# Kernel tuning notes

Measured on AMD Instinct MI355X. Metric: run time of the kernel, lower is better.

Reference implementation:

```python
import jax, jax.numpy as jnp
import numpy as np

IN_DIM = 128
OUT_DIM = 128
NUM_HEADS = 4
HEAD_DIM = OUT_DIM // NUM_HEADS  # 32
B, N = 4, 4096


def setup_inputs() -> dict:
    key = jax.random.key(0)
    ks = jax.random.split(key, 7)
    s_in = 1.0 / np.sqrt(IN_DIM)
    s_out = 1.0 / np.sqrt(OUT_DIM)
    return {
        "x": jax.random.normal(ks[0], (B, N, IN_DIM), dtype=jnp.float32),
        "adjacency": jax.random.randint(ks[1], (N, N), 0, 2, dtype=jnp.int32),
        "W_q": jax.random.uniform(ks[2], (IN_DIM, NUM_HEADS * HEAD_DIM), jnp.float32, -s_in, s_in),
        "W_k": jax.random.uniform(ks[3], (IN_DIM, NUM_HEADS * HEAD_DIM), jnp.float32, -s_in, s_in),
        "W_v": jax.random.uniform(ks[4], (IN_DIM, NUM_HEADS * HEAD_DIM), jnp.float32, -s_in, s_in),
        "W_o": jax.random.uniform(ks[5], (OUT_DIM, OUT_DIM), jnp.float32, -s_out, s_out),
        "b_o": jax.random.uniform(ks[6], (OUT_DIM,), jnp.float32, -s_out, s_out),
    }


def reference(x, adjacency, W_q, W_k, W_v, W_o, b_o):
    Bn, Nn, _ = x.shape
    # QKV projections -> (B, H, N, Dh)
    q = (x @ W_q).reshape(Bn, Nn, NUM_HEADS, HEAD_DIM).transpose(0, 2, 1, 3)
    k = (x @ W_k).reshape(Bn, Nn, NUM_HEADS, HEAD_DIM).transpose(0, 2, 1, 3)
    v = (x @ W_v).reshape(Bn, Nn, NUM_HEADS, HEAD_DIM).transpose(0, 2, 1, 3)
    scores = jnp.einsum("bhnd,bhmd->bhnm", q, k) / np.sqrt(HEAD_DIM).astype(np.float32)
    # adjacency mask (1,1,N,N): -inf where no edge
    adj = adjacency[None, None, :, :]
    scores = jnp.where(adj == 0, -jnp.inf, scores)
    attn = jax.nn.softmax(scores, axis=-1)
    out = jnp.einsum("bhnm,bhmd->bhnd", attn, v)
    out = out.transpose(0, 2, 1, 3).reshape(Bn, Nn, NUM_HEADS * HEAD_DIM)  # concat heads
    return out @ W_o + b_o
```

## Files before the change

### kernel.cpp

```cpp
#include <hip/hip_runtime.h>
#include <stdint.h>

typedef __attribute__((ext_vector_type(4))) short short4v;
typedef __attribute__((ext_vector_type(8))) short bf16x8;
typedef __attribute__((ext_vector_type(4))) float f32x4;
typedef __attribute__((ext_vector_type(2))) uint32_t uint2v;
typedef __attribute__((ext_vector_type(4))) uint32_t uint4v;
typedef __attribute__((ext_vector_type(4))) uint16_t ushort4v;

#define NN 4096

__device__ __forceinline__ uint16_t f2bf(float f) {
    union { float f; uint32_t u; } c; c.f = f;
    uint32_t r = c.u + 0x7FFF + ((c.u >> 16) & 1);
    return (uint16_t)(r >> 16);
}

__global__ __launch_bounds__(256) void pack_kernel(
    const int* __restrict__ adj, uint64_t* __restrict__ bits,
    const float* __restrict__ Wq, const float* __restrict__ Wk,
    const float* __restrict__ Wv, const float* __restrict__ Wo,
    uint16_t* __restrict__ WT, uint16_t* __restrict__ WoT)
{
    const int lane = threadIdx.x & 63;
    const int wave = (blockIdx.x * blockDim.x + threadIdx.x) >> 6;
    const int nwaves = (gridDim.x * blockDim.x) >> 6;
    const int TOT = (NN * NN) / 64;
    for (int i = wave; i < TOT; i += nwaves) {
        int v = adj[(size_t)i * 64 + lane];
        uint64_t m = __ballot(v != 0);
        if (lane == 0) bits[i] = m;
    }
    const int tid = blockIdx.x * blockDim.x + threadIdx.x;
    const int nth = gridDim.x * blockDim.x;
    for (int t = tid; t < 3 * 128 * 128 + 128 * 128; t += nth) {
        if (t < 3 * 128 * 128) {
            int j = t >> 7, k = t & 127;
            int m = j >> 7, jj = j & 127;
            const float* W = (m == 0) ? Wq : ((m == 1) ? Wk : Wv);
            float v = W[k * 128 + jj];
            if (m == 0) v *= (0.17677669529663687f * 1.4426950408889634f);
            WT[t] = f2bf(v);
        } else {
            int t2 = t - 3 * 128 * 128;
            int j = t2 >> 7, k = t2 & 127;
            WoT[t2] = f2bf(Wo[k * 128 + j]);
        }
    }
}

__global__ __launch_bounds__(256) void qkv_kernel(
    const float* __restrict__ x, const uint16_t* __restrict__ WT,
    uint16_t* __restrict__ Q, uint16_t* __restrict__ Kf, uint16_t* __restrict__ Vf)
{
    const int wave = threadIdx.x >> 6, lane = threadIdx.x & 63;
    const int g = lane >> 4, l15 = lane & 15;
    const int ntile = blockIdx.x * 4 + wave;
    const int n = ntile * 16 + l15;
    const int b = n >> 12, nn = n & 4095;

    const char* xrow = (const char*)x + (size_t)n * 512;
    bf16x8 xb[4];
#pragma unroll
    for (int ks = 0; ks < 4; ++ks) {
        f32x4 a = *(const f32x4*)(xrow + ks * 128 + g * 16);
        f32x4 c = *(const f32x4*)(xrow + ks * 128 + 64 + g * 16);
        bf16x8 f;
#pragma unroll
        for (int i = 0; i < 4; ++i) { f[i] = (short)f2bf(a[i]); f[4 + i] = (short)f2bf(c[i]); }
        xb[ks] = f;
    }

#pragma unroll 1
    for (int jt = 0; jt < 24; ++jt) {
        const int j0 = jt * 16;
        const char* wrow = (const char*)WT + (size_t)(j0 + l15) * 256;
        f32x4 acc = {0.f, 0.f, 0.f, 0.f};
#pragma unroll
        for (int ks = 0; ks < 4; ++ks) {
            short4v a0 = *(const short4v*)(wrow + ks * 64 + g * 8);
            short4v a1 = *(const short4v*)(wrow + ks * 64 + 32 + g * 8);
            bf16x8 af = __builtin_shufflevector(a0, a1, 0, 1, 2, 3, 4, 5, 6, 7);
            acc = __builtin_amdgcn_mfma_f32_16x16x32_bf16(af, xb[ks], acc, 0, 0, 0);
        }
        const int m = j0 >> 7;
        const int bh = b * 4 + ((j0 & 127) >> 5);
        if (m == 0) {
            const int d0 = (j0 & 31) + g * 4;
            ushort4v st;
#pragma unroll
            for (int r = 0; r < 4; ++r) st[r] = f2bf(acc[r]);
            *(ushort4v*)(Q + ((size_t)bh * 4096 + nn) * 32 + d0) = st;
        } else if (m == 1) {
            const int half = (j0 >> 4) & 1;
            ushort4v st;
#pragma unroll
            for (int r = 0; r < 4; ++r) st[r] = f2bf(acc[r]);
            *(ushort4v*)(Kf + ((size_t)bh << 17) + (ntile & 255) * 512 + lane * 8 + half * 4) = st;
        } else {
            const int half = (j0 >> 4) & 1;
            uint16_t* vb2 = Vf + ((size_t)bh << 17) + ((ntile & 255) >> 1) * 1024 + half * 512
                          + ((l15 >> 2) * 16 + g * 4) * 8 + (l15 & 3) + ((ntile & 1) << 2);
#pragma unroll
            for (int r = 0; r < 4; ++r) vb2[r * 8] = f2bf(acc[r]);
        }
    }
}

__global__ __launch_bounds__(256) void attn_kernel(
    const uint16_t* __restrict__ Q, const uint16_t* __restrict__ Kf,
    const uint16_t* __restrict__ Vf, const uint32_t* __restrict__ bits,
    uint16_t* __restrict__ O)
{
    __shared__ f32x4 cmb[4][4][2][64];
    __shared__ float csum[4][4][64];
    const int tid = threadIdx.x;
    const int wave = tid >> 6, lane = tid & 63;
    const int g = lane >> 4, l15 = lane & 15, gsh = g * 4;
    const int blk = blockIdx.x;
    const int bh = ((blk & 7) << 1) | ((blk >> 3) & 1);
    const int qb = blk >> 4;
    const int q0 = qb * 64;

    const char* Kp = (const char*)Kf + ((size_t)bh << 18) + wave * 65536 + lane * 16;
    const char* Vp = (const char*)Vf + ((size_t)bh << 18) + wave * 65536 + lane * 16;
    const uint32_t* ap[4];
#pragma unroll
    for (int qg = 0; qg < 4; ++qg)
        ap[qg] = bits + (size_t)(q0 + qg * 16 + l15) * 128 + wave * 32;

    bf16x8 qf[4];
#pragma unroll
    for (int qg = 0; qg < 4; ++qg) {
        const char* qrow = (const char*)Q + ((size_t)bh * 4096 + q0 + qg * 16 + l15) * 64;
        short4v a0 = *(const short4v*)(qrow + g * 8);
        short4v a1 = *(const short4v*)(qrow + 32 + g * 8);
        qf[qg] = __builtin_shufflevector(a0, a1, 0, 1, 2, 3, 4, 5, 6, 7);
    }

    bf16x8 ones;
#pragma unroll
    for (int i = 0; i < 8; ++i) ones[i] = (short)0x3F80;

    const f32x4 z = {0.f, 0.f, 0.f, 0.f};
    f32x4 o[4][2], sacc[4];
#pragma unroll
    for (int qg = 0; qg < 4; ++qg) { o[qg][0] = z; o[qg][1] = z; sacc[qg] = z; }

    bf16x8 kc[4], kn[4];
    uint2v wc[4], wn[4];
#pragma unroll
    for (int j = 0; j < 4; ++j) kc[j] = *(const bf16x8*)(Kp + j * 1024);
    Kp += 4096;
#pragma unroll
    for (int qg = 0; qg < 4; ++qg) { wc[qg] = *(const uint2v*)ap[qg]; ap[qg] += 2; }

    auto body = [&](bf16x8 (&kcur)[4], uint2v (&wcur)[4],
                    bf16x8 (&knxt)[4], uint2v (&wnxt)[4]) {
#pragma unroll
        for (int j = 0; j < 4; ++j) knxt[j] = *(const bf16x8*)(Kp + j * 1024);
        Kp += 4096;
#pragma unroll
        for (int qg = 0; qg < 4; ++qg) { wnxt[qg] = *(const uint2v*)ap[qg]; ap[qg] += 2; }
        bf16x8 vc[4];
#pragma unroll
        for (int i = 0; i < 4; ++i) vc[i] = *(const bf16x8*)(Vp + i * 1024);
        Vp += 4096;

#pragma unroll
        for (int qg = 0; qg < 4; ++qg) {
            f32x4 s[4];
#pragma unroll
            for (int j = 0; j < 4; ++j)
                s[j] = __builtin_amdgcn_mfma_f32_16x16x32_bf16(kcur[j], qf[qg], z, 0, 0, 0);
            float p[16];
#pragma unroll
            for (int j = 0; j < 4; ++j) {
                uint32_t wj = wcur[qg][j >> 1] >> (((j & 1) << 4) + gsh);
#pragma unroll
                for (int r = 0; r < 4; ++r) {
                    float pv = __builtin_amdgcn_exp2f(s[j][r]);
                    int msk = ((int)(wj << (31 - r))) >> 31;
                    p[j * 4 + r] = __uint_as_float(__float_as_uint(pv) & (uint32_t)msk);
                }
            }
            uint32_t pk[8];
#pragma unroll
            for (int i = 0; i < 8; ++i) {
                uint32_t r_;
                asm("v_cvt_pk_bf16_f32 %0, %1, %2" : "=v"(r_) : "v"(p[2 * i]), "v"(p[2 * i + 1]));
                pk[i] = r_;
            }
            uint4v u0 = {pk[0], pk[1], pk[2], pk[3]};
            uint4v u1 = {pk[4], pk[5], pk[6], pk[7]};
            bf16x8 pf0 = __builtin_bit_cast(bf16x8, u0);
            bf16x8 pf1 = __builtin_bit_cast(bf16x8, u1);
            o[qg][0] = __builtin_amdgcn_mfma_f32_16x16x32_bf16(vc[0], pf0, o[qg][0], 0, 0, 0);
            o[qg][0] = __builtin_amdgcn_mfma_f32_16x16x32_bf16(vc[2], pf1, o[qg][0], 0, 0, 0);
            o[qg][1] = __builtin_amdgcn_mfma_f32_16x16x32_bf16(vc[1], pf0, o[qg][1], 0, 0, 0);
            o[qg][1] = __builtin_amdgcn_mfma_f32_16x16x32_bf16(vc[3], pf1, o[qg][1], 0, 0, 0);
            sacc[qg] = __builtin_amdgcn_mfma_f32_16x16x32_bf16(ones, pf0, sacc[qg], 0, 0, 0);
            sacc[qg] = __builtin_amdgcn_mfma_f32_16x16x32_bf16(ones, pf1, sacc[qg], 0, 0, 0);
        }
    };

#pragma unroll 1
    for (int tt = 0; tt < 16; tt += 2) {
        body(kc, wc, kn, wn);
        body(kn, wn, kc, wc);
    }

#pragma unroll
    for (int qg = 0; qg < 4; ++qg) {
        cmb[wave][qg][0][lane] = o[qg][0];
        cmb[wave][qg][1][lane] = o[qg][1];
        csum[wave][qg][lane] = sacc[qg][0];
    }
    __syncthreads();
    {
        const int qg = wave;
        f32x4 a0 = cmb[0][qg][0][lane];
        f32x4 a1 = cmb[0][qg][1][lane];
        float sd = csum[0][qg][lane];
#pragma unroll
        for (int v = 1; v < 4; ++v) {
            a0 += cmb[v][qg][0][lane];
            a1 += cmb[v][qg][1][lane];
            sd += csum[v][qg][lane];
        }
        const float inv = 1.0f / sd;
        const int q = q0 + qg * 16 + l15;
        uint16_t* orow = O + ((size_t)bh * 4096 + q) * 32;
        ushort4v st0, st1;
#pragma unroll
        for (int r = 0; r < 4; ++r) {
            st0[r] = f2bf(a0[r] * inv);
            st1[r] = f2bf(a1[r] * inv);
        }
        *(ushort4v*)(orow + gsh) = st0;
        *(ushort4v*)(orow + 16 + gsh) = st1;
    }
}

__global__ __launch_bounds__(256) void proj_kernel(
    const uint16_t* __restrict__ A, const uint16_t* __restrict__ WoT,
    const float* __restrict__ bo, float* __restrict__ out)
{
    const int wave = threadIdx.x >> 6, lane = threadIdx.x & 63;
    const int g = lane >> 4, l15 = lane & 15;
    const int ntile = blockIdx.x * 4 + wave;
    const int n = ntile * 16 + l15;
    const int b = n >> 12, nn = n & 4095;

    bf16x8 bfr[4];
#pragma unroll
    for (int h = 0; h < 4; ++h) {
        const char* arow = (const char*)A + (((size_t)(b * 4 + h)) * 4096 + nn) * 64;
        short4v a0 = *(const short4v*)(arow + g * 8);
        short4v a1 = *(const short4v*)(arow + 32 + g * 8);
        bfr[h] = __builtin_shufflevector(a0, a1, 0, 1, 2, 3, 4, 5, 6, 7);
    }
#pragma unroll 1
    for (int ct = 0; ct < 8; ++ct) {
        const int c0 = ct * 16;
        const char* wrow = (const char*)WoT + (size_t)(c0 + l15) * 256;
        f32x4 acc = {0.f, 0.f, 0.f, 0.f};
#pragma unroll
        for (int h = 0; h < 4; ++h) {
            short4v a0 = *(const short4v*)(wrow + h * 64 + g * 8);
            short4v a1 = *(const short4v*)(wrow + h * 64 + 32 + g * 8);
            bf16x8 af = __builtin_shufflevector(a0, a1, 0, 1, 2, 3, 4, 5, 6, 7);
            acc = __builtin_amdgcn_mfma_f32_16x16x32_bf16(af, bfr[h], acc, 0, 0, 0);
        }
        f32x4 bias = *(const f32x4*)(bo + c0 + g * 4);
#pragma unroll
        for (int r = 0; r < 4; ++r) acc[r] += bias[r];
        *(f32x4*)(out + (size_t)n * 128 + c0 + g * 4) = acc;
    }
}

extern "C" void kernel_launch(void* const* d_in, const int* in_sizes, int n_in,
                              void* d_out, int out_size, void* d_ws, size_t ws_size,
                              hipStream_t stream)
{
    const float* x   = (const float*)d_in[0];
    const int*   adj = (const int*)d_in[1];
    const float* Wq  = (const float*)d_in[2];
    const float* Wk  = (const float*)d_in[3];
    const float* Wv  = (const float*)d_in[4];
    const float* Wo  = (const float*)d_in[5];
    const float* bo  = (const float*)d_in[6];
    float* out = (float*)d_out;

    char* ws = (char*)d_ws;
    uint16_t* Q    = (uint16_t*)(ws);
    uint16_t* Kf   = (uint16_t*)(ws + ((size_t)4 << 20));
    uint16_t* Vf   = (uint16_t*)(ws + ((size_t)8 << 20));
    uint16_t* AO   = (uint16_t*)(ws + ((size_t)12 << 20));
    uint32_t* bits = (uint32_t*)(ws + ((size_t)16 << 20));
    uint16_t* WT   = (uint16_t*)(ws + ((size_t)18 << 20));
    uint16_t* WoT  = (uint16_t*)(ws + ((size_t)18 << 20) + 98304);

    hipLaunchKernelGGL(pack_kernel, dim3(2048), dim3(256), 0, stream,
                       adj, (uint64_t*)bits, Wq, Wk, Wv, Wo, WT, WoT);
    hipLaunchKernelGGL(qkv_kernel, dim3(256), dim3(256), 0, stream,
                       x, WT, Q, Kf, Vf);
    hipLaunchKernelGGL(attn_kernel, dim3(1024), dim3(256), 0, stream,
                       Q, Kf, Vf, bits, AO);
    hipLaunchKernelGGL(proj_kernel, dim3(256), dim3(256), 0, stream,
                       AO, WoT, bo, out);
}
```

Before: 125.9 us.

## Overlap adjacency bit-packing with QKV projection and widen QKV and proj grids

Splits weight packing into its own small kernel and merges the adjacency bit-packing into the QKV kernel as extra blocks, so the memory-bound adjacency scan runs alongside the projection GEMM. QKV now uses one block per matrix (Q/K/V) per row tile and the output projection splits the columns across four times as many blocks, to fill more CUs. V is computed with swapped MFMA operands so its stores become vectorised. The attention kernel also gets s_setprio around its MFMA groups to favour matrix issue. The fused QKV kernel recomputes the x bf16 conversion three times per row tile.

```diff
diff --git a/kernel.cpp b/kernel.cpp
--- a/kernel.cpp
+++ b/kernel.cpp
@@ -16,46 +16,63 @@
     return (uint16_t)(r >> 16);
 }
 
-__global__ __launch_bounds__(256) void pack_kernel(
-    const int* __restrict__ adj, uint64_t* __restrict__ bits,
+__global__ __launch_bounds__(256) void wpack_kernel(
     const float* __restrict__ Wq, const float* __restrict__ Wk,
     const float* __restrict__ Wv, const float* __restrict__ Wo,
     uint16_t* __restrict__ WT, uint16_t* __restrict__ WoT)
 {
-    const int lane = threadIdx.x & 63;
-    const int wave = (blockIdx.x * blockDim.x + threadIdx.x) >> 6;
-    const int nwaves = (gridDim.x * blockDim.x) >> 6;
-    const int TOT = (NN * NN) / 64;
-    for (int i = wave; i < TOT; i += nwaves) {
-        int v = adj[(size_t)i * 64 + lane];
-        uint64_t m = __ballot(v != 0);
-        if (lane == 0) bits[i] = m;
-    }
-    const int tid = blockIdx.x * blockDim.x + threadIdx.x;
-    const int nth = gridDim.x * blockDim.x;
-    for (int t = tid; t < 3 * 128 * 128 + 128 * 128; t += nth) {
-        if (t < 3 * 128 * 128) {
-            int j = t >> 7, k = t & 127;
-            int m = j >> 7, jj = j & 127;
-            const float* W = (m == 0) ? Wq : ((m == 1) ? Wk : Wv);
-            float v = W[k * 128 + jj];
-            if (m == 0) v *= (0.17677669529663687f * 1.4426950408889634f);
-            WT[t] = f2bf(v);
-        } else {
-            int t2 = t - 3 * 128 * 128;
-            int j = t2 >> 7, k = t2 & 127;
-            WoT[t2] = f2bf(Wo[k * 128 + j]);
-        }
-    }
-}
-
-__global__ __launch_bounds__(256) void qkv_kernel(
+    const int t = blockIdx.x * 256 + threadIdx.x;
+    if (t < 3 * 128 * 128) {
+        int j = t >> 7, k = t & 127;
+        int m = j >> 7, jj = j & 127;
+        const float* W = (m == 0) ? Wq : ((m == 1) ? Wk : Wv);
+        float v = W[k * 128 + jj];
+        if (m == 0) v *= (0.17677669529663687f * 1.4426950408889634f);
+        WT[t] = f2bf(v);
+    } else {
+        int t2 = t - 3 * 128 * 128;
+        int j = t2 >> 7, k = t2 & 127;
+        WoT[t2] = f2bf(Wo[k * 128 + j]);
+    }
+}
+
+__global__ __launch_bounds__(256) void adjqkv_kernel(
+    const int* __restrict__ adj, uint64_t* __restrict__ bits,
     const float* __restrict__ x, const uint16_t* __restrict__ WT,
     uint16_t* __restrict__ Q, uint16_t* __restrict__ Kf, uint16_t* __restrict__ Vf)
 {
-    const int wave = threadIdx.x >> 6, lane = threadIdx.x & 63;
+    const int blk = blockIdx.x;
+    const int tid = threadIdx.x;
+    const int wave = tid >> 6, lane = tid & 63;
+
+    if (blk >= 768) {
+        const int ablk = blk - 768;
+        const int wid = (ablk * 256 + tid) >> 6;
+        const int base = wid * 32;
+        const int* src = adj + (size_t)base * 64 + lane;
+#pragma unroll 1
+        for (int ii = 0; ii < 32; ii += 4) {
+            int v0 = src[(ii + 0) * 64];
+            int v1 = src[(ii + 1) * 64];
+            int v2 = src[(ii + 2) * 64];
+            int v3 = src[(ii + 3) * 64];
+            uint64_t m0 = __ballot(v0 != 0);
+            uint64_t m1 = __ballot(v1 != 0);
+            uint64_t m2 = __ballot(v2 != 0);
+            uint64_t m3 = __ballot(v3 != 0);
+            if (lane == 0) {
+                bits[base + ii + 0] = m0;
+                bits[base + ii + 1] = m1;
+                bits[base + ii + 2] = m2;
+                bits[base + ii + 3] = m3;
+            }
+        }
+        return;
+    }
+
     const int g = lane >> 4, l15 = lane & 15;
-    const int ntile = blockIdx.x * 4 + wave;
+    const int m = blk >> 8;
+    const int ntile = (blk & 255) * 4 + wave;
     const int n = ntile * 16 + l15;
     const int b = n >> 12, nn = n & 4095;
 
@@ -72,8 +89,9 @@
     }
 
 #pragma unroll 1
-    for (int jt = 0; jt < 24; ++jt) {
+    for (int jt = m * 8; jt < m * 8 + 8; ++jt) {
         const int j0 = jt * 16;
+        const bool isV = (m == 2);
         const char* wrow = (const char*)WT + (size_t)(j0 + l15) * 256;
         f32x4 acc = {0.f, 0.f, 0.f, 0.f};
 #pragma unroll
@@ -81,28 +99,22 @@
             short4v a0 = *(const short4v*)(wrow + ks * 64 + g * 8);
             short4v a1 = *(const short4v*)(wrow + ks * 64 + 32 + g * 8);
             bf16x8 af = __builtin_shufflevector(a0, a1, 0, 1, 2, 3, 4, 5, 6, 7);
-            acc = __builtin_amdgcn_mfma_f32_16x16x32_bf16(af, xb[ks], acc, 0, 0, 0);
-        }
-        const int m = j0 >> 7;
+            acc = isV ? __builtin_amdgcn_mfma_f32_16x16x32_bf16(xb[ks], af, acc, 0, 0, 0)
+                      : __builtin_amdgcn_mfma_f32_16x16x32_bf16(af, xb[ks], acc, 0, 0, 0);
+        }
         const int bh = b * 4 + ((j0 & 127) >> 5);
+        const int half = (j0 >> 4) & 1;
+        ushort4v st;
+#pragma unroll
+        for (int r = 0; r < 4; ++r) st[r] = f2bf(acc[r]);
         if (m == 0) {
             const int d0 = (j0 & 31) + g * 4;
-            ushort4v st;
-#pragma unroll
-            for (int r = 0; r < 4; ++r) st[r] = f2bf(acc[r]);
             *(ushort4v*)(Q + ((size_t)bh * 4096 + nn) * 32 + d0) = st;
         } else if (m == 1) {
-            const int half = (j0 >> 4) & 1;
-            ushort4v st;
-#pragma unroll
-            for (int r = 0; r < 4; ++r) st[r] = f2bf(acc[r]);
             *(ushort4v*)(Kf + ((size_t)bh << 17) + (ntile & 255) * 512 + lane * 8 + half * 4) = st;
         } else {
-            const int half = (j0 >> 4) & 1;
-            uint16_t* vb2 = Vf + ((size_t)bh << 17) + ((ntile & 255) >> 1) * 1024 + half * 512
-                          + ((l15 >> 2) * 16 + g * 4) * 8 + (l15 & 3) + ((ntile & 1) << 2);
-#pragma unroll
-            for (int r = 0; r < 4; ++r) vb2[r * 8] = f2bf(acc[r]);
+            *(ushort4v*)(Vf + ((size_t)bh << 17) + ((ntile & 255) >> 1) * 1024
+                         + half * 512 + lane * 8 + ((ntile & 1) << 2)) = st;
         }
     }
 }
@@ -170,9 +182,11 @@
 #pragma unroll
         for (int qg = 0; qg < 4; ++qg) {
             f32x4 s[4];
+            __builtin_amdgcn_s_setprio(1);
 #pragma unroll
             for (int j = 0; j < 4; ++j)
                 s[j] = __builtin_amdgcn_mfma_f32_16x16x32_bf16(kcur[j], qf[qg], z, 0, 0, 0);
+            __builtin_amdgcn_s_setprio(0);
             float p[16];
 #pragma unroll
             for (int j = 0; j < 4; ++j) {
@@ -195,12 +209,14 @@
             uint4v u1 = {pk[4], pk[5], pk[6], pk[7]};
             bf16x8 pf0 = __builtin_bit_cast(bf16x8, u0);
             bf16x8 pf1 = __builtin_bit_cast(bf16x8, u1);
+            __builtin_amdgcn_s_setprio(1);
             o[qg][0] = __builtin_amdgcn_mfma_f32_16x16x32_bf16(vc[0], pf0, o[qg][0], 0, 0, 0);
             o[qg][0] = __builtin_amdgcn_mfma_f32_16x16x32_bf16(vc[2], pf1, o[qg][0], 0, 0, 0);
             o[qg][1] = __builtin_amdgcn_mfma_f32_16x16x32_bf16(vc[1], pf0, o[qg][1], 0, 0, 0);
             o[qg][1] = __builtin_amdgcn_mfma_f32_16x16x32_bf16(vc[3], pf1, o[qg][1], 0, 0, 0);
             sacc[qg] = __builtin_amdgcn_mfma_f32_16x16x32_bf16(ones, pf0, sacc[qg], 0, 0, 0);
             sacc[qg] = __builtin_amdgcn_mfma_f32_16x16x32_bf16(ones, pf1, sacc[qg], 0, 0, 0);
+            __builtin_amdgcn_s_setprio(0);
         }
     };
 
@@ -248,7 +264,9 @@
 {
     const int wave = threadIdx.x >> 6, lane = threadIdx.x & 63;
     const int g = lane >> 4, l15 = lane & 15;
-    const int ntile = blockIdx.x * 4 + wave;
+    const int blk = blockIdx.x;
+    const int ctbase = (blk >> 8) * 2;
+    const int ntile = (blk & 255) * 4 + wave;
     const int n = ntile * 16 + l15;
     const int b = n >> 12, nn = n & 4095;
 
@@ -261,7 +279,7 @@
         bfr[h] = __builtin_shufflevector(a0, a1, 0, 1, 2, 3, 4, 5, 6, 7);
     }
 #pragma unroll 1
-    for (int ct = 0; ct < 8; ++ct) {
+    for (int ct = ctbase; ct < ctbase + 2; ++ct) {
         const int c0 = ct * 16;
         const char* wrow = (const char*)WoT + (size_t)(c0 + l15) * 256;
         f32x4 acc = {0.f, 0.f, 0.f, 0.f};
@@ -301,12 +319,12 @@
     uint16_t* WT   = (uint16_t*)(ws + ((size_t)18 << 20));
     uint16_t* WoT  = (uint16_t*)(ws + ((size_t)18 << 20) + 98304);
 
-    hipLaunchKernelGGL(pack_kernel, dim3(2048), dim3(256), 0, stream,
-                       adj, (uint64_t*)bits, Wq, Wk, Wv, Wo, WT, WoT);
-    hipLaunchKernelGGL(qkv_kernel, dim3(256), dim3(256), 0, stream,
-                       x, WT, Q, Kf, Vf);
+    hipLaunchKernelGGL(wpack_kernel, dim3(256), dim3(256), 0, stream,
+                       Wq, Wk, Wv, Wo, WT, WoT);
+    hipLaunchKernelGGL(adjqkv_kernel, dim3(2816), dim3(256), 0, stream,
+                       adj, (uint64_t*)bits, x, WT, Q, Kf, Vf);
     hipLaunchKernelGGL(attn_kernel, dim3(1024), dim3(256), 0, stream,
                        Q, Kf, Vf, bits, AO);
-    hipLaunchKernelGGL(proj_kernel, dim3(256), dim3(256), 0, stream,
+    hipLaunchKernelGGL(proj_kernel, dim3(1024), dim3(256), 0, stream,
                        AO, WoT, bo, out);
 }
```

New measurement: 123.3 us. -2.0%, faster.
